# Optimization experiments

Hardware: AMD Instinct MI355X
Metric: run time of the kernel (lower is better)

The kernel has to match this reference:

```python
import jax, jax.numpy as jnp
import numpy as np
from jax import lax

EPROJS, DUNITS, ATT_DIM = 512, 1024, 320
ACONV_CHANS, ACONV_FILTS = 10, 100
B, T = 64, 2048
SCALING = 2.0


def setup_inputs() -> dict:
    key = jax.random.key(0)
    ks = jax.random.split(key, 10)
    enc_hs_pad = jax.random.normal(ks[0], (B, T, EPROJS), dtype=jnp.float32)
    # lengths in [T//2, T] so no row is fully masked
    enc_hs_len = jax.random.randint(ks[1], (B,), T // 2, T + 1).astype(jnp.int32)
    dec_z = jax.random.normal(ks[2], (B, DUNITS), dtype=jnp.float32)
    att_prev = jax.random.uniform(ks[3], (B, T), dtype=jnp.float32)
    # normalize att_prev like a prob. distribution over valid frames
    att_prev = att_prev / jnp.sum(att_prev, axis=1, keepdims=True)
    s = 0.02
    W_enc = jax.random.normal(ks[4], (ATT_DIM, EPROJS), dtype=jnp.float32) * s
    b_enc = jnp.zeros((ATT_DIM,), dtype=jnp.float32)
    W_dec = jax.random.normal(ks[5], (ATT_DIM, DUNITS), dtype=jnp.float32) * s
    W_att = jax.random.normal(ks[6], (ATT_DIM, ACONV_CHANS), dtype=jnp.float32) * s
    # Conv2d(1, aconv_chans, (1, 2*filts+1)) acts as 1D conv over time
    conv_w = jax.random.normal(ks[7], (ACONV_CHANS, 1, 2 * ACONV_FILTS + 1), dtype=jnp.float32) * s
    W_g = jax.random.normal(ks[8], (1, ATT_DIM), dtype=jnp.float32) * s
    b_g = jnp.zeros((1,), dtype=jnp.float32)
    return {
        "enc_hs_pad": enc_hs_pad, "enc_hs_len": enc_hs_len, "dec_z": dec_z,
        "att_prev": att_prev, "W_enc": W_enc, "b_enc": b_enc, "W_dec": W_dec,
        "W_att": W_att, "conv_w": conv_w, "W_g": W_g, "b_g": b_g,
    }


def reference(enc_hs_pad, enc_hs_len, dec_z, att_prev,
              W_enc, b_enc, W_dec, W_att, conv_w, W_g, b_g):
    # pre_compute_enc_h = mlp_enc(enc_h): [B, T, att_dim]
    pre_enc = jnp.einsum('bte,ae->bta', enc_hs_pad, W_enc) + b_enc
    # location conv: att_prev [B, T] -> [B, C, T] (SAME padding)
    att_conv = lax.conv_general_dilated(
        att_prev[:, None, :], conv_w, window_strides=(1,),
        padding=[(ACONV_FILTS, ACONV_FILTS)],
        dimension_numbers=('NCH', 'OIH', 'NCH'))
    # mlp_att over channels: [B, T, att_dim]
    att_feat = jnp.einsum('bct,ac->bta', att_conv, W_att)
    # mlp_dec(dec_z): [B, 1, att_dim]
    dec_feat = (dec_z @ W_dec.T)[:, None, :]
    # energies: gvec(tanh(sum)) -> [B, T]
    e = jnp.einsum('bta,a->bt', jnp.tanh(att_feat + pre_enc + dec_feat), W_g[0]) + b_g[0]
    # mask padded frames
    t_idx = jnp.arange(e.shape[1])
    pad_mask = t_idx[None, :] >= enc_hs_len[:, None]
    e = jnp.where(pad_mask, -jnp.inf, e)
    w = jax.nn.softmax(SCALING * e, axis=1)
    # context: weighted sum over encoder states -> [B, D_enc]
    c = jnp.einsum('bte,bt->be', enc_hs_pad, w)
    return (c, w)
```

## Files before the change

kernel.cpp:

```cpp
#include <hip/hip_runtime.h>
#include <hip/hip_bf16.h>

#define B_SZ 64
#define T_SZ 2048
#define EPROJS 512
#define DUNITS 1024
#define ATT_DIM 320
#define NCH 10
#define KFILT 201
#define PAD 100

typedef __attribute__((ext_vector_type(8))) __bf16 bf16x8;
typedef __attribute__((ext_vector_type(4))) float f32x4;
typedef __attribute__((ext_vector_type(8))) unsigned short u16x8;

__device__ __forceinline__ unsigned short f2b(float f) {
    __bf16 h = (__bf16)f;
    return __builtin_bit_cast(unsigned short, h);
}

__global__ void cvt_wenc(const float* __restrict__ W, unsigned short* __restrict__ out) {
    int i = (blockIdx.x * 256 + threadIdx.x) * 4;
    float4 v = *(const float4*)(W + i);
    ushort4 o;
    o.x = f2b(v.x); o.y = f2b(v.y); o.z = f2b(v.z); o.w = f2b(v.w);
    *(ushort4*)(out + i) = o;
}

__global__ void dec_feat_k(const float* __restrict__ dec_z, const float* __restrict__ W_dec,
                           const float* __restrict__ b_enc, float* __restrict__ df) {
    int b = blockIdx.x;
    int a = threadIdx.x;
    const float4* z = (const float4*)(dec_z + b * DUNITS);
    const float4* w = (const float4*)(W_dec + (size_t)a * DUNITS);
    float s = b_enc[a];
    #pragma unroll 4
    for (int d = 0; d < DUNITS / 4; ++d) {
        float4 zv = z[d], wv = w[d];
        s += zv.x * wv.x + zv.y * wv.y + zv.z * wv.z + zv.w * wv.w;
    }
    df[b * ATT_DIM + a] = s;
}

__global__ void conv_k(const float* __restrict__ ap, const float* __restrict__ cw,
                       float* __restrict__ out) {
    int b = blockIdx.x, c = blockIdx.y;
    __shared__ float s_ap[T_SZ];
    __shared__ float s_cw[KFILT];
    int tid = threadIdx.x;
    for (int i = tid; i < T_SZ; i += 256) s_ap[i] = ap[b * T_SZ + i];
    for (int i = tid; i < KFILT; i += 256) s_cw[i] = cw[c * KFILT + i];
    __syncthreads();
    for (int j = 0; j < T_SZ / 256; ++j) {
        int t = tid + j * 256;
        int klo = max(0, PAD - t);
        int khi = min(KFILT, T_SZ + PAD - t);
        float s = 0.f;
        for (int k = klo; k < khi; ++k) s += s_ap[t - PAD + k] * s_cw[k];
        out[((size_t)(b * NCH + c)) * T_SZ + t] = s;
    }
}

__global__ __launch_bounds__(512, 1) void energy_k(
    const float* __restrict__ enc, const unsigned short* __restrict__ wbf,
    const float* __restrict__ df, const float* __restrict__ att_conv,
    const float* __restrict__ W_att, const float* __restrict__ W_g,
    float* __restrict__ e_out)
{
    __shared__ unsigned short sW[ATT_DIM * 64];
    __shared__ float sDf[ATT_DIM], sWg[ATT_DIM], sWatt[ATT_DIM * NCH], sConv[NCH * 128];

    int tid = threadIdx.x;
    int lane = tid & 63, wave = tid >> 6;
    int blk = blockIdx.x;
    int b = blk >> 4;
    int t0 = (blk & 15) << 7;

    for (int i = tid; i < ATT_DIM; i += 512) { sDf[i] = df[b * ATT_DIM + i]; sWg[i] = W_g[i]; }
    for (int i = tid; i < ATT_DIM * NCH; i += 512) sWatt[i] = W_att[i];
    for (int i = tid; i < NCH * 128; i += 512)
        sConv[i] = att_conv[((size_t)(b * NCH + (i >> 7))) * T_SZ + t0 + (i & 127)];

    f32x4 acc[20];
    #pragma unroll
    for (int n = 0; n < 20; ++n) acc[n] = (f32x4){0.f, 0.f, 0.f, 0.f};

    int m15 = lane & 15, kg = lane >> 4;
    int row = t0 + wave * 16 + m15;
    const float* aP = enc + ((size_t)b * T_SZ + row) * EPROJS;

    for (int k0 = 0; k0 < EPROJS; k0 += 64) {
        __syncthreads();
        #pragma unroll
        for (int r = 0; r < 5; ++r) {
            int idx = r * 512 + tid;
            int wr = idx >> 3, k8 = idx & 7;
            u16x8 v = *(const u16x8*)(wbf + (size_t)wr * EPROJS + k0 + k8 * 8);
            int k8s = k8 ^ (wr & 7);
            *(u16x8*)(sW + wr * 64 + k8s * 8) = v;
        }
        __syncthreads();
        #pragma unroll
        for (int kk = 0; kk < 2; ++kk) {
            const float4 a0 = *(const float4*)(aP + k0 + kk * 32 + kg * 8);
            const float4 a1 = *(const float4*)(aP + k0 + kk * 32 + kg * 8 + 4);
            bf16x8 af;
            af[0] = (__bf16)a0.x; af[1] = (__bf16)a0.y; af[2] = (__bf16)a0.z; af[3] = (__bf16)a0.w;
            af[4] = (__bf16)a1.x; af[5] = (__bf16)a1.y; af[6] = (__bf16)a1.z; af[7] = (__bf16)a1.w;
            int k8r = kk * 4 + kg;
            #pragma unroll
            for (int nt = 0; nt < 20; ++nt) {
                int wr = nt * 16 + m15;
                bf16x8 wf = *(const bf16x8*)(sW + wr * 64 + ((k8r ^ (wr & 7)) * 8));
                acc[nt] = __builtin_amdgcn_mfma_f32_16x16x32_bf16(af, wf, acc[nt], 0, 0, 0);
            }
        }
    }

    int tl_base = wave * 16 + kg * 4;
    #pragma unroll
    for (int r = 0; r < 4; ++r) {
        int tl = tl_base + r;
        float s = 0.f;
        #pragma unroll
        for (int nt = 0; nt < 20; ++nt) {
            int col = nt * 16 + m15;
            float v = acc[nt][r] + sDf[col];
            float afeat = 0.f;
            #pragma unroll
            for (int c = 0; c < NCH; ++c) afeat += sWatt[col * NCH + c] * sConv[c * 128 + tl];
            v += afeat;
            v = fminf(fmaxf(v, -15.f), 15.f);
            float e2 = __expf(2.f * v);
            s += sWg[col] * ((e2 - 1.f) / (e2 + 1.f));
        }
        s += __shfl_xor(s, 1); s += __shfl_xor(s, 2);
        s += __shfl_xor(s, 4); s += __shfl_xor(s, 8);
        if (m15 == 0) e_out[b * T_SZ + t0 + tl] = s;
    }
}

__global__ void softmax_k(const float* __restrict__ e, const int* __restrict__ len,
                          float* __restrict__ w_out, float* __restrict__ w_ws) {
    int b = blockIdx.x, tid = threadIdx.x;
    int lane = tid & 63, wave = tid >> 6;
    int L = len[b];
    float ev[8];
    float m = -1e30f;
    #pragma unroll
    for (int i = 0; i < 8; ++i) {
        int t = tid + i * 256;
        float x = e[b * T_SZ + t];
        if (t >= L) x = -1e30f;
        ev[i] = x;
        m = fmaxf(m, x);
    }
    #pragma unroll
    for (int o = 32; o > 0; o >>= 1) m = fmaxf(m, __shfl_xor(m, o));
    __shared__ float sred[4];
    if (lane == 0) sred[wave] = m;
    __syncthreads();
    m = fmaxf(fmaxf(sred[0], sred[1]), fmaxf(sred[2], sred[3]));

    float ex[8];
    float sum = 0.f;
    #pragma unroll
    for (int i = 0; i < 8; ++i) { ex[i] = __expf(2.f * (ev[i] - m)); sum += ex[i]; }
    #pragma unroll
    for (int o = 32; o > 0; o >>= 1) sum += __shfl_xor(sum, o);
    __shared__ float sred2[4];
    if (lane == 0) sred2[wave] = sum;
    __syncthreads();
    sum = sred2[0] + sred2[1] + sred2[2] + sred2[3];
    float inv = 1.f / sum;
    #pragma unroll
    for (int i = 0; i < 8; ++i) {
        int t = tid + i * 256;
        float w = ex[i] * inv;
        w_out[b * T_SZ + t] = w;
        w_ws[b * T_SZ + t] = w;
    }
}

__global__ void ctx_partial_k(const float* __restrict__ enc, const float* __restrict__ w,
                              float* __restrict__ part) {
    int b = blockIdx.x, tc = blockIdx.y, tid = threadIdx.x;
    int half = tid >> 7;
    int c4 = tid & 127;
    f32x4 s = (f32x4){0.f, 0.f, 0.f, 0.f};
    int tb = tc * 128;
    #pragma unroll 4
    for (int i = half; i < 128; i += 2) {
        float wv = w[b * T_SZ + tb + i];
        f32x4 v = *(const f32x4*)(enc + ((size_t)b * T_SZ + tb + i) * EPROJS + c4 * 4);
        s += wv * v;
    }
    *(f32x4*)(part + ((size_t)(b * 32 + tc * 2 + half)) * EPROJS + c4 * 4) = s;
}

__global__ void ctx_reduce_k(const float* __restrict__ part, float* __restrict__ c_out) {
    int b = blockIdx.x;
    int c4 = threadIdx.x;
    f32x4 s = (f32x4){0.f, 0.f, 0.f, 0.f};
    #pragma unroll
    for (int tc = 0; tc < 32; ++tc)
        s += *(const f32x4*)(part + ((size_t)(b * 32 + tc)) * EPROJS + c4 * 4);
    *(f32x4*)(c_out + b * EPROJS + c4 * 4) = s;
}

extern "C" void kernel_launch(void* const* d_in, const int* in_sizes, int n_in,
                              void* d_out, int out_size, void* d_ws, size_t ws_size,
                              hipStream_t stream) {
    const float* enc      = (const float*)d_in[0];
    const int*   len      = (const int*)d_in[1];
    const float* dec_z    = (const float*)d_in[2];
    const float* att_prev = (const float*)d_in[3];
    const float* W_enc    = (const float*)d_in[4];
    const float* b_enc    = (const float*)d_in[5];
    const float* W_dec    = (const float*)d_in[6];
    const float* W_att    = (const float*)d_in[7];
    const float* conv_w   = (const float*)d_in[8];
    const float* W_g      = (const float*)d_in[9];

    char* ws = (char*)d_ws;
    size_t off = 0;
    unsigned short* wbf = (unsigned short*)(ws + off); off += (size_t)ATT_DIM * EPROJS * 2;
    float* e_buf  = (float*)(ws + off); off += (size_t)B_SZ * T_SZ * 4;
    float* dfb    = (float*)(ws + off); off += (size_t)B_SZ * ATT_DIM * 4;
    float* att_cv = (float*)(ws + off); off += (size_t)B_SZ * NCH * T_SZ * 4;
    float* w_ws   = (float*)(ws + off); off += (size_t)B_SZ * T_SZ * 4;
    float* part   = (float*)(ws + off); off += (size_t)B_SZ * 32 * EPROJS * 4;

    float* c_out = (float*)d_out;
    float* w_out = (float*)d_out + B_SZ * EPROJS;

    cvt_wenc<<<dim3(160), dim3(256), 0, stream>>>(W_enc, wbf);
    dec_feat_k<<<dim3(B_SZ), dim3(ATT_DIM), 0, stream>>>(dec_z, W_dec, b_enc, dfb);
    conv_k<<<dim3(B_SZ, NCH), dim3(256), 0, stream>>>(att_prev, conv_w, att_cv);
    energy_k<<<dim3(B_SZ * 16), dim3(512), 0, stream>>>(enc, wbf, dfb, att_cv, W_att, W_g, e_buf);
    softmax_k<<<dim3(B_SZ), dim3(256), 0, stream>>>(e_buf, len, w_out, w_ws);
    ctx_partial_k<<<dim3(B_SZ, 16), dim3(256), 0, stream>>>(enc, w_ws, part);
    ctx_reduce_k<<<dim3(B_SZ), dim3(128), 0, stream>>>(part, c_out);
}
```

Measured before the change: 250.6 us.

## Prefetch encoder tiles in energy kernel, skip masked frames in context, drop w copy

The energy kernel now issues the global loads for the next K-chunk of encoder rows before the shared-memory barrier, hiding load latency behind the MFMA loop of the current chunk. The context kernel skips loading encoder rows whose softmax weight is zero, which avoids reading the padded frames beyond each sequence length. The softmax no longer writes a duplicate workspace copy of the weights, and the context kernel reads the output weights directly. These changes add register pressure from the prefetch and a data-dependent branch in the context loop.

```diff
diff --git a/kernel.cpp b/kernel.cpp
--- a/kernel.cpp
+++ b/kernel.cpp
@@ -76,6 +76,15 @@
     int b = blk >> 4;
     int t0 = (blk & 15) << 7;
 
+    int m15 = lane & 15, kg = lane >> 4;
+    int row = t0 + wave * 16 + m15;
+    const float* aP = enc + ((size_t)b * T_SZ + row) * EPROJS;
+
+    float4 a0 = *(const float4*)(aP + kg * 8);
+    float4 a1 = *(const float4*)(aP + kg * 8 + 4);
+    float4 a2 = *(const float4*)(aP + 32 + kg * 8);
+    float4 a3 = *(const float4*)(aP + 32 + kg * 8 + 4);
+
     for (int i = tid; i < ATT_DIM; i += 512) { sDf[i] = df[b * ATT_DIM + i]; sWg[i] = W_g[i]; }
     for (int i = tid; i < ATT_DIM * NCH; i += 512) sWatt[i] = W_att[i];
     for (int i = tid; i < NCH * 128; i += 512)
@@ -84,10 +93,6 @@
     f32x4 acc[20];
     #pragma unroll
     for (int n = 0; n < 20; ++n) acc[n] = (f32x4){0.f, 0.f, 0.f, 0.f};
-
-    int m15 = lane & 15, kg = lane >> 4;
-    int row = t0 + wave * 16 + m15;
-    const float* aP = enc + ((size_t)b * T_SZ + row) * EPROJS;
 
     for (int k0 = 0; k0 < EPROJS; k0 += 64) {
         __syncthreads();
@@ -99,22 +104,32 @@
             int k8s = k8 ^ (wr & 7);
             *(u16x8*)(sW + wr * 64 + k8s * 8) = v;
         }
+        int kn = (k0 + 64) & (EPROJS - 1);
+        float4 n0 = *(const float4*)(aP + kn + kg * 8);
+        float4 n1 = *(const float4*)(aP + kn + kg * 8 + 4);
+        float4 n2 = *(const float4*)(aP + kn + 32 + kg * 8);
+        float4 n3 = *(const float4*)(aP + kn + 32 + kg * 8 + 4);
         __syncthreads();
-        #pragma unroll
-        for (int kk = 0; kk < 2; ++kk) {
-            const float4 a0 = *(const float4*)(aP + k0 + kk * 32 + kg * 8);
-            const float4 a1 = *(const float4*)(aP + k0 + kk * 32 + kg * 8 + 4);
-            bf16x8 af;
-            af[0] = (__bf16)a0.x; af[1] = (__bf16)a0.y; af[2] = (__bf16)a0.z; af[3] = (__bf16)a0.w;
-            af[4] = (__bf16)a1.x; af[5] = (__bf16)a1.y; af[6] = (__bf16)a1.z; af[7] = (__bf16)a1.w;
-            int k8r = kk * 4 + kg;
-            #pragma unroll
-            for (int nt = 0; nt < 20; ++nt) {
-                int wr = nt * 16 + m15;
-                bf16x8 wf = *(const bf16x8*)(sW + wr * 64 + ((k8r ^ (wr & 7)) * 8));
-                acc[nt] = __builtin_amdgcn_mfma_f32_16x16x32_bf16(af, wf, acc[nt], 0, 0, 0);
-            }
-        }
+
+        bf16x8 af0, af1;
+        af0[0] = (__bf16)a0.x; af0[1] = (__bf16)a0.y; af0[2] = (__bf16)a0.z; af0[3] = (__bf16)a0.w;
+        af0[4] = (__bf16)a1.x; af0[5] = (__bf16)a1.y; af0[6] = (__bf16)a1.z; af0[7] = (__bf16)a1.w;
+        af1[0] = (__bf16)a2.x; af1[1] = (__bf16)a2.y; af1[2] = (__bf16)a2.z; af1[3] = (__bf16)a2.w;
+        af1[4] = (__bf16)a3.x; af1[5] = (__bf16)a3.y; af1[6] = (__bf16)a3.z; af1[7] = (__bf16)a3.w;
+
+        #pragma unroll
+        for (int nt = 0; nt < 20; ++nt) {
+            int wr = nt * 16 + m15;
+            bf16x8 wf0 = *(const bf16x8*)(sW + wr * 64 + ((kg ^ (wr & 7)) * 8));
+            acc[nt] = __builtin_amdgcn_mfma_f32_16x16x32_bf16(af0, wf0, acc[nt], 0, 0, 0);
+        }
+        #pragma unroll
+        for (int nt = 0; nt < 20; ++nt) {
+            int wr = nt * 16 + m15;
+            bf16x8 wf1 = *(const bf16x8*)(sW + wr * 64 + (((4 + kg) ^ (wr & 7)) * 8));
+            acc[nt] = __builtin_amdgcn_mfma_f32_16x16x32_bf16(af1, wf1, acc[nt], 0, 0, 0);
+        }
+        a0 = n0; a1 = n1; a2 = n2; a3 = n3;
     }
 
     int tl_base = wave * 16 + kg * 4;
@@ -141,7 +156,7 @@
 }
 
 __global__ void softmax_k(const float* __restrict__ e, const int* __restrict__ len,
-                          float* __restrict__ w_out, float* __restrict__ w_ws) {
+                          float* __restrict__ w_out) {
     int b = blockIdx.x, tid = threadIdx.x;
     int lane = tid & 63, wave = tid >> 6;
     int L = len[b];
@@ -176,9 +191,7 @@
     #pragma unroll
     for (int i = 0; i < 8; ++i) {
         int t = tid + i * 256;
-        float w = ex[i] * inv;
-        w_out[b * T_SZ + t] = w;
-        w_ws[b * T_SZ + t] = w;
+        w_out[b * T_SZ + t] = ex[i] * inv;
     }
 }
 
@@ -189,11 +202,12 @@
     int c4 = tid & 127;
     f32x4 s = (f32x4){0.f, 0.f, 0.f, 0.f};
     int tb = tc * 128;
-    #pragma unroll 4
     for (int i = half; i < 128; i += 2) {
         float wv = w[b * T_SZ + tb + i];
-        f32x4 v = *(const f32x4*)(enc + ((size_t)b * T_SZ + tb + i) * EPROJS + c4 * 4);
-        s += wv * v;
+        if (wv != 0.f) {
+            f32x4 v = *(const f32x4*)(enc + ((size_t)b * T_SZ + tb + i) * EPROJS + c4 * 4);
+            s += wv * v;
+        }
     }
     *(f32x4*)(part + ((size_t)(b * 32 + tc * 2 + half)) * EPROJS + c4 * 4) = s;
 }
@@ -228,7 +242,6 @@
     float* e_buf  = (float*)(ws + off); off += (size_t)B_SZ * T_SZ * 4;
     float* dfb    = (float*)(ws + off); off += (size_t)B_SZ * ATT_DIM * 4;
     float* att_cv = (float*)(ws + off); off += (size_t)B_SZ * NCH * T_SZ * 4;
-    float* w_ws   = (float*)(ws + off); off += (size_t)B_SZ * T_SZ * 4;
     float* part   = (float*)(ws + off); off += (size_t)B_SZ * 32 * EPROJS * 4;
 
     float* c_out = (float*)d_out;
@@ -238,7 +251,7 @@
     dec_feat_k<<<dim3(B_SZ), dim3(ATT_DIM), 0, stream>>>(dec_z, W_dec, b_enc, dfb);
     conv_k<<<dim3(B_SZ, NCH), dim3(256), 0, stream>>>(att_prev, conv_w, att_cv);
     energy_k<<<dim3(B_SZ * 16), dim3(512), 0, stream>>>(enc, wbf, dfb, att_cv, W_att, W_g, e_buf);
-    softmax_k<<<dim3(B_SZ), dim3(256), 0, stream>>>(e_buf, len, w_out, w_ws);
-    ctx_partial_k<<<dim3(B_SZ, 16), dim3(256), 0, stream>>>(enc, w_ws, part);
+    softmax_k<<<dim3(B_SZ), dim3(256), 0, stream>>>(e_buf, len, w_out);
+    ctx_partial_k<<<dim3(B_SZ, 16), dim3(256), 0, stream>>>(enc, w_out, part);
     ctx_reduce_k<<<dim3(B_SZ), dim3(128), 0, stream>>>(part, c_out);
 }
```

Result: slower. 274.0 us (+9.4%).
